# Performance work log

Hardware: AMD Instinct MI355X
Metric: run time of the kernel (lower is better)

Reference implementation:

```python
import jax, jax.numpy as jnp
import numpy as np

TEMPERATURE = 0.07
N_CLASSES = 100


def setup_inputs() -> dict:
    key = jax.random.key(0)
    k1, k2 = jax.random.split(key)
    N, D = 8192, 128
    emb = jax.random.normal(k1, (N, D), dtype=jnp.float32)
    # unit-normalize so exp(sim / temperature) stays finite in fp32
    emb = emb / jnp.linalg.norm(emb, axis=1, keepdims=True)
    labels = jax.random.randint(k2, (N,), 0, N_CLASSES, dtype=jnp.int64)
    return {"embeddings": emb, "labels": labels}


def reference(embeddings, labels):
    N = embeddings.shape[0]
    dt = embeddings.dtype
    # [N, N] similarity
    sim = jnp.matmul(embeddings, embeddings.T) / TEMPERATURE
    off_diag = 1.0 - jnp.eye(N, dtype=dt)
    pos_mask = (labels[:, None] == labels[None, :]).astype(dt) * off_diag
    exp_sim = jnp.exp(sim) * off_diag  # diagonal zeroed
    positive_sum = jnp.sum(exp_sim * pos_mask, axis=1)
    total_sum = jnp.sum(exp_sim, axis=1)
    loss = -jnp.log(positive_sum / (total_sum + 1e-8) + 1e-8)
    valid = pos_mask.sum(axis=1) > 0
    cnt = jnp.sum(valid.astype(dt))
    mean_loss = jnp.where(
        cnt > 0,
        jnp.sum(jnp.where(valid, loss, jnp.zeros_like(loss))) / jnp.maximum(cnt, 1.0),
        jnp.asarray(0.0, dtype=dt),
    )
    return mean_loss
```

## Files before the change

kernel.cpp:

```cpp
#include <hip/hip_runtime.h>

#define N 8192
#define D 128
#define SCALE_A 20.6098592f
#define NBX 128
#define NBY 8
#define NBLK (NBX * NBY)
#define ITERS 8

using short8  = __attribute__((ext_vector_type(8))) short;
using float4v = __attribute__((ext_vector_type(4))) float;

#if __has_builtin(__builtin_amdgcn_exp2f)
#define EXP2(x) __builtin_amdgcn_exp2f(x)
#else
#define EXP2(x) __expf((x) * 0.69314718f)
#endif

static __device__ inline unsigned int f2bf(float f) {
    union { float f; unsigned int u; } x;
    x.f = f;
    unsigned int u = x.u;
    return (u + 0x7FFFu + ((u >> 16) & 1u)) >> 16;
}

__global__ __launch_bounds__(256) void cl_prep(
    const float* __restrict__ emb, unsigned short* __restrict__ bfB,
    unsigned short* __restrict__ bfA, float* __restrict__ tot,
    int* __restrict__ ticket)
{
    const int t = blockIdx.x * 256 + threadIdx.x;
    const float* p = emb + (size_t)t * 16;
    uint4 ob[2], oa[2];
    #pragma unroll
    for (int h = 0; h < 2; ++h) {
        float4v f0 = *(const float4v*)(p + h * 8);
        float4v f1 = *(const float4v*)(p + h * 8 + 4);
        ob[h].x = f2bf(f0[0]) | (f2bf(f0[1]) << 16);
        ob[h].y = f2bf(f0[2]) | (f2bf(f0[3]) << 16);
        ob[h].z = f2bf(f1[0]) | (f2bf(f1[1]) << 16);
        ob[h].w = f2bf(f1[2]) | (f2bf(f1[3]) << 16);
        oa[h].x = f2bf(f0[0] * SCALE_A) | (f2bf(f0[1] * SCALE_A) << 16);
        oa[h].y = f2bf(f0[2] * SCALE_A) | (f2bf(f0[3] * SCALE_A) << 16);
        oa[h].z = f2bf(f1[0] * SCALE_A) | (f2bf(f1[1] * SCALE_A) << 16);
        oa[h].w = f2bf(f1[2] * SCALE_A) | (f2bf(f1[3] * SCALE_A) << 16);
    }
    ((uint4*)bfB)[t * 2]     = ob[0];
    ((uint4*)bfB)[t * 2 + 1] = ob[1];
    ((uint4*)bfA)[t * 2]     = oa[0];
    ((uint4*)bfA)[t * 2 + 1] = oa[1];
    if (t < 2 * N) tot[t] = 0.f;
    if (t == 0) *ticket = 0;
}

static __device__ __forceinline__ void stage_tile(
    const uint4* __restrict__ bfB4, int cbase, uint4* lds_dst, int tid)
{
    const uint4* src = bfB4 + (size_t)cbase * 16;
    #pragma unroll
    for (int i = 0; i < 8; ++i) {
        const int g     = tid + i * 256;
        const int row   = g >> 4;
        const int chunk = g & 15;
        __builtin_amdgcn_global_load_lds(
            (const __attribute__((address_space(1))) void*)(src + row * 16 + (chunk ^ (row & 15))),
            (__attribute__((address_space(3))) void*)(lds_dst + g),
            16, 0, 0);
    }
}

__global__ __launch_bounds__(256, 4) void cl_main(
    const unsigned short* __restrict__ bfA, const unsigned short* __restrict__ bfB,
    const int* __restrict__ labels,
    float* __restrict__ tot, float* __restrict__ pos,
    int* __restrict__ ticket, float* __restrict__ out)
{
    __shared__ uint4 ldsB[128 * 16];
    __shared__ int   s_collab[1024];
    __shared__ float sred[2][4];
    __shared__ int   s_ticket;

    const int tid  = threadIdx.x;
    const int lane = tid & 63;
    const int wave = tid >> 6;
    const int q    = lane >> 4;
    const int c    = lane & 15;
    const int rw     = blockIdx.x * 64 + wave * 16;
    const int cbase0 = blockIdx.y * 1024;
    const uint4* bfB4 = (const uint4*)bfB;

    stage_tile(bfB4, cbase0, &ldsB[0], tid);

    short8 afrag[4];
    int rowlab[4];
    {
        const int arow = rw + c;
        #pragma unroll
        for (int ks = 0; ks < 4; ++ks)
            afrag[ks] = *(const short8*)(bfA + (size_t)arow * D + ks * 32 + q * 8);
        #pragma unroll
        for (int reg = 0; reg < 4; ++reg)
            rowlab[reg] = labels[rw + q * 4 + reg];
    }

    {
        int4 lv = *(const int4*)(labels + cbase0 + tid * 4);
        *(int4*)(&s_collab[tid * 4]) = lv;
    }
    asm volatile("s_waitcnt vmcnt(0) lgkmcnt(0)" ::: "memory");
    __builtin_amdgcn_s_barrier();
    __builtin_amdgcn_sched_barrier(0);

    float tot_a[4] = {0.f, 0.f, 0.f, 0.f};
    float pos_a[4] = {0.f, 0.f, 0.f, 0.f};

    #pragma unroll 1
    for (int it = 0; it < ITERS; ++it) {
        const int cbase = cbase0 + it * 128;

        float4v acc[8];
        #pragma unroll
        for (int tc = 0; tc < 8; ++tc) {
            float4v z = {0.f, 0.f, 0.f, 0.f};
            acc[tc] = z;
        }

        const short8* ldsS = (const short8*)ldsB;
        #pragma unroll
        for (int ks = 0; ks < 4; ++ks) {
            const short8* pk = ldsS + c * 16 + ((ks * 4 + q) ^ c);
            #pragma unroll
            for (int tc = 0; tc < 8; ++tc) {
                short8 b = pk[tc * 256];
                acc[tc] = __builtin_amdgcn_mfma_f32_16x16x32_bf16(
                    afrag[ks], b, acc[tc], 0, 0, 0);
            }
        }

        #pragma unroll
        for (int tc = 0; tc < 8; ++tc) {
            const bool diag_tile = (rw == cbase + tc * 16);
            const int lc = s_collab[it * 128 + tc * 16 + c];
            #pragma unroll
            for (int reg = 0; reg < 4; ++reg) {
                float v = EXP2(acc[tc][reg]);
                if (diag_tile && (q * 4 + reg) == c) v = 0.f;
                tot_a[reg] += v;
                if (rowlab[reg] == lc) pos_a[reg] += v;
            }
        }

        __builtin_amdgcn_sched_barrier(0);
        __builtin_amdgcn_s_barrier();
        __builtin_amdgcn_sched_barrier(0);

        if (it < ITERS - 1) {
            stage_tile(bfB4, cbase0 + (it + 1) * 128, &ldsB[0], tid);
            asm volatile("s_waitcnt vmcnt(0)" ::: "memory");
            __builtin_amdgcn_s_barrier();
            __builtin_amdgcn_sched_barrier(0);
        }
    }

    #pragma unroll
    for (int reg = 0; reg < 4; ++reg) {
        float t = tot_a[reg];
        float p = pos_a[reg];
        #pragma unroll
        for (int m = 1; m < 16; m <<= 1) {
            t += __shfl_xor(t, m, 64);
            p += __shfl_xor(p, m, 64);
        }
        if (c == 0) {
            const int r = rw + q * 4 + reg;
            atomicAdd(&tot[r], t);
            atomicAdd(&pos[r], p);
        }
    }

    asm volatile("s_waitcnt vmcnt(0)" ::: "memory");
    __syncthreads();
    if (tid == 0)
        s_ticket = __hip_atomic_fetch_add(ticket, 1, __ATOMIC_RELAXED,
                                          __HIP_MEMORY_SCOPE_AGENT);
    __syncthreads();
    if (s_ticket != NBLK - 1) return;

    float lsum = 0.f, lcnt = 0.f;
    #pragma unroll 4
    for (int i = tid; i < N; i += 256) {
        const float t = __hip_atomic_load(&tot[i], __ATOMIC_RELAXED,
                                          __HIP_MEMORY_SCOPE_AGENT);
        const float p = __hip_atomic_load(&pos[i], __ATOMIC_RELAXED,
                                          __HIP_MEMORY_SCOPE_AGENT);
        const float loss = -__logf(p / (t + 1e-8f) + 1e-8f);
        if (p > 0.f) { lsum += loss; lcnt += 1.f; }
    }
    #pragma unroll
    for (int m = 1; m < 64; m <<= 1) {
        lsum += __shfl_xor(lsum, m, 64);
        lcnt += __shfl_xor(lcnt, m, 64);
    }
    if (lane == 0) { sred[0][wave] = lsum; sred[1][wave] = lcnt; }
    __syncthreads();
    if (tid == 0) {
        const float s = sred[0][0] + sred[0][1] + sred[0][2] + sred[0][3];
        const float n = sred[1][0] + sred[1][1] + sred[1][2] + sred[1][3];
        out[0] = (n > 0.f) ? s / fmaxf(n, 1.f) : 0.f;
    }
}

extern "C" void kernel_launch(void* const* d_in, const int* in_sizes, int n_in,
                              void* d_out, int out_size, void* d_ws, size_t ws_size,
                              hipStream_t stream) {
    const float* emb  = (const float*)d_in[0];
    const int* labels = (const int*)d_in[1];
    unsigned short* bfB = (unsigned short*)d_ws;
    unsigned short* bfA = bfB + (size_t)N * D;
    float* tot    = (float*)(bfA + (size_t)N * D);
    float* pos    = tot + N;
    int*   ticket = (int*)(pos + N);

    cl_prep<<<256, 256, 0, stream>>>(emb, bfB, bfA, tot, ticket);
    cl_main<<<dim3(NBX, NBY), 256, 0, stream>>>(bfA, bfB, labels, tot, pos,
                                                ticket, (float*)d_out);
}
```

Before: 93.91 us.

## Exploit similarity symmetry with upper-triangular block tiling and column-side accumulation

Since the similarity matrix is symmetric, only upper-triangular 128x128 blocks are computed, each by one 512-thread block. Every exp value is added to both its row sums and its column sums. On diagonal blocks, tiles below the wave's diagonal are skipped and the lower triangle inside the diagonal tile is masked. This roughly halves the MFMA and exp work, at the cost of more atomics (both row and column) and the loss of the per-block multi-iteration reuse of the A fragments. There is also a slightly different rounding order from the asymmetric bf16 scaling, because the A operand is pre-scaled while the B operand is not, so the sim values used for column sums come from the same product.

```diff
diff --git a/kernel.cpp b/kernel.cpp
--- a/kernel.cpp
+++ b/kernel.cpp
@@ -3,10 +3,8 @@
 #define N 8192
 #define D 128
 #define SCALE_A 20.6098592f
-#define NBX 128
-#define NBY 8
-#define NBLK (NBX * NBY)
-#define ITERS 8
+#define NP 64
+#define NBLK (NP * (NP + 1) / 2)
 
 using short8  = __attribute__((ext_vector_type(8))) short;
 using float4v = __attribute__((ext_vector_type(4))) float;
@@ -53,31 +51,14 @@
     if (t == 0) *ticket = 0;
 }
 
-static __device__ __forceinline__ void stage_tile(
-    const uint4* __restrict__ bfB4, int cbase, uint4* lds_dst, int tid)
-{
-    const uint4* src = bfB4 + (size_t)cbase * 16;
-    #pragma unroll
-    for (int i = 0; i < 8; ++i) {
-        const int g     = tid + i * 256;
-        const int row   = g >> 4;
-        const int chunk = g & 15;
-        __builtin_amdgcn_global_load_lds(
-            (const __attribute__((address_space(1))) void*)(src + row * 16 + (chunk ^ (row & 15))),
-            (__attribute__((address_space(3))) void*)(lds_dst + g),
-            16, 0, 0);
-    }
-}
-
-__global__ __launch_bounds__(256, 4) void cl_main(
+__global__ __launch_bounds__(512, 4) void cl_main(
     const unsigned short* __restrict__ bfA, const unsigned short* __restrict__ bfB,
     const int* __restrict__ labels,
     float* __restrict__ tot, float* __restrict__ pos,
     int* __restrict__ ticket, float* __restrict__ out)
 {
     __shared__ uint4 ldsB[128 * 16];
-    __shared__ int   s_collab[1024];
-    __shared__ float sred[2][4];
+    __shared__ float sred[2][8];
     __shared__ int   s_ticket;
 
     const int tid  = threadIdx.x;
@@ -85,80 +66,88 @@
     const int wave = tid >> 6;
     const int q    = lane >> 4;
     const int c    = lane & 15;
-    const int rw     = blockIdx.x * 64 + wave * 16;
-    const int cbase0 = blockIdx.y * 1024;
-    const uint4* bfB4 = (const uint4*)bfB;
-
-    stage_tile(bfB4, cbase0, &ldsB[0], tid);
+
+    const int k = blockIdx.x;
+    int bi = (int)((129.0f - sqrtf(16641.0f - 8.0f * (float)k)) * 0.5f);
+    while (bi * (129 - bi) / 2 > k) --bi;
+    while ((bi + 1) * (128 - bi) / 2 <= k) ++bi;
+    const int bj = bi + (k - bi * (129 - bi) / 2);
+    const int R0 = bi * 128, C0 = bj * 128;
+    const bool diagblk = (bi == bj);
+
+    const uint4* src = (const uint4*)bfB + (size_t)C0 * 16;
+    #pragma unroll
+    for (int i = 0; i < 4; ++i) {
+        const int g     = tid + i * 512;
+        const int row   = g >> 4;
+        const int chunk = g & 15;
+        __builtin_amdgcn_global_load_lds(
+            (const __attribute__((address_space(1))) void*)(src + row * 16 + (chunk ^ (row & 15))),
+            (__attribute__((address_space(3))) void*)(&ldsB[g]),
+            16, 0, 0);
+    }
 
     short8 afrag[4];
-    int rowlab[4];
+    int rowlab[4], collab[8];
     {
-        const int arow = rw + c;
+        const int arow = R0 + wave * 16 + c;
         #pragma unroll
         for (int ks = 0; ks < 4; ++ks)
             afrag[ks] = *(const short8*)(bfA + (size_t)arow * D + ks * 32 + q * 8);
         #pragma unroll
         for (int reg = 0; reg < 4; ++reg)
-            rowlab[reg] = labels[rw + q * 4 + reg];
-    }
-
-    {
-        int4 lv = *(const int4*)(labels + cbase0 + tid * 4);
-        *(int4*)(&s_collab[tid * 4]) = lv;
-    }
-    asm volatile("s_waitcnt vmcnt(0) lgkmcnt(0)" ::: "memory");
+            rowlab[reg] = labels[R0 + wave * 16 + q * 4 + reg];
+        #pragma unroll
+        for (int tc = 0; tc < 8; ++tc)
+            collab[tc] = labels[C0 + tc * 16 + c];
+    }
+
+    asm volatile("s_waitcnt vmcnt(0)" ::: "memory");
     __builtin_amdgcn_s_barrier();
     __builtin_amdgcn_sched_barrier(0);
 
+    float4v acc[8];
+    #pragma unroll
+    for (int tc = 0; tc < 8; ++tc) {
+        float4v z = {0.f, 0.f, 0.f, 0.f};
+        acc[tc] = z;
+    }
+    const short8* ldsS = (const short8*)ldsB;
+    #pragma unroll
+    for (int ks = 0; ks < 4; ++ks) {
+        const short8* pk = ldsS + c * 16 + ((ks * 4 + q) ^ c);
+        #pragma unroll
+        for (int tc = 0; tc < 8; ++tc) {
+            if (diagblk && tc < wave) continue;
+            short8 b = pk[tc * 256];
+            acc[tc] = __builtin_amdgcn_mfma_f32_16x16x32_bf16(
+                afrag[ks], b, acc[tc], 0, 0, 0);
+        }
+    }
+
     float tot_a[4] = {0.f, 0.f, 0.f, 0.f};
     float pos_a[4] = {0.f, 0.f, 0.f, 0.f};
-
-    #pragma unroll 1
-    for (int it = 0; it < ITERS; ++it) {
-        const int cbase = cbase0 + it * 128;
-
-        float4v acc[8];
-        #pragma unroll
-        for (int tc = 0; tc < 8; ++tc) {
-            float4v z = {0.f, 0.f, 0.f, 0.f};
-            acc[tc] = z;
-        }
-
-        const short8* ldsS = (const short8*)ldsB;
-        #pragma unroll
-        for (int ks = 0; ks < 4; ++ks) {
-            const short8* pk = ldsS + c * 16 + ((ks * 4 + q) ^ c);
-            #pragma unroll
-            for (int tc = 0; tc < 8; ++tc) {
-                short8 b = pk[tc * 256];
-                acc[tc] = __builtin_amdgcn_mfma_f32_16x16x32_bf16(
-                    afrag[ks], b, acc[tc], 0, 0, 0);
-            }
-        }
-
-        #pragma unroll
-        for (int tc = 0; tc < 8; ++tc) {
-            const bool diag_tile = (rw == cbase + tc * 16);
-            const int lc = s_collab[it * 128 + tc * 16 + c];
+    float ctot[8]  = {0.f, 0.f, 0.f, 0.f, 0.f, 0.f, 0.f, 0.f};
+    float cpos[8]  = {0.f, 0.f, 0.f, 0.f, 0.f, 0.f, 0.f, 0.f};
+    #pragma unroll
+    for (int tc = 0; tc < 8; ++tc) {
+        if (diagblk && tc < wave) continue;
+        const int lc = collab[tc];
+        if (diagblk && tc == wave) {
             #pragma unroll
             for (int reg = 0; reg < 4; ++reg) {
                 float v = EXP2(acc[tc][reg]);
-                if (diag_tile && (q * 4 + reg) == c) v = 0.f;
-                tot_a[reg] += v;
-                if (rowlab[reg] == lc) pos_a[reg] += v;
+                if ((q * 4 + reg) >= c) v = 0.f;
+                tot_a[reg] += v;  ctot[tc] += v;
+                if (rowlab[reg] == lc) { pos_a[reg] += v; cpos[tc] += v; }
             }
-        }
-
-        __builtin_amdgcn_sched_barrier(0);
-        __builtin_amdgcn_s_barrier();
-        __builtin_amdgcn_sched_barrier(0);
-
-        if (it < ITERS - 1) {
-            stage_tile(bfB4, cbase0 + (it + 1) * 128, &ldsB[0], tid);
-            asm volatile("s_waitcnt vmcnt(0)" ::: "memory");
-            __builtin_amdgcn_s_barrier();
-            __builtin_amdgcn_sched_barrier(0);
+        } else {
+            #pragma unroll
+            for (int reg = 0; reg < 4; ++reg) {
+                float v = EXP2(acc[tc][reg]);
+                tot_a[reg] += v;  ctot[tc] += v;
+                if (rowlab[reg] == lc) { pos_a[reg] += v; cpos[tc] += v; }
+            }
         }
     }
 
@@ -172,9 +161,22 @@
             p += __shfl_xor(p, m, 64);
         }
         if (c == 0) {
-            const int r = rw + q * 4 + reg;
+            const int r = R0 + wave * 16 + q * 4 + reg;
             atomicAdd(&tot[r], t);
             atomicAdd(&pos[r], p);
+        }
+    }
+
+    #pragma unroll
+    for (int tc = 0; tc < 8; ++tc) {
+        if (diagblk && tc < wave) continue;
+        float t = ctot[tc], p = cpos[tc];
+        t += __shfl_xor(t, 16, 64);  t += __shfl_xor(t, 32, 64);
+        p += __shfl_xor(p, 16, 64);  p += __shfl_xor(p, 32, 64);
+        if (q == 0) {
+            const int cc = C0 + tc * 16 + c;
+            atomicAdd(&tot[cc], t);
+            atomicAdd(&pos[cc], p);
         }
     }
 
@@ -188,7 +190,7 @@
 
     float lsum = 0.f, lcnt = 0.f;
     #pragma unroll 4
-    for (int i = tid; i < N; i += 256) {
+    for (int i = tid; i < N; i += 512) {
         const float t = __hip_atomic_load(&tot[i], __ATOMIC_RELAXED,
                                           __HIP_MEMORY_SCOPE_AGENT);
         const float p = __hip_atomic_load(&pos[i], __ATOMIC_RELAXED,
@@ -204,8 +206,9 @@
     if (lane == 0) { sred[0][wave] = lsum; sred[1][wave] = lcnt; }
     __syncthreads();
     if (tid == 0) {
-        const float s = sred[0][0] + sred[0][1] + sred[0][2] + sred[0][3];
-        const float n = sred[1][0] + sred[1][1] + sred[1][2] + sred[1][3];
+        float s = 0.f, n = 0.f;
+        #pragma unroll
+        for (int w = 0; w < 8; ++w) { s += sred[0][w]; n += sred[1][w]; }
         out[0] = (n > 0.f) ? s / fmaxf(n, 1.f) : 0.f;
     }
 }
@@ -222,6 +225,6 @@
     int*   ticket = (int*)(pos + N);
 
     cl_prep<<<256, 256, 0, stream>>>(emb, bfB, bfA, tot, ticket);
-    cl_main<<<dim3(NBX, NBY), 256, 0, stream>>>(bfA, bfB, labels, tot, pos,
-                                                ticket, (float*)d_out);
-}
+    cl_main<<<NBLK, 512, 0, stream>>>(bfA, bfB, labels, tot, pos,
+                                      ticket, (float*)d_out);
+}
```

Measured after the change: 114.2 us. 1.22x slower.
